# Kernel optimization log

Measured on AMD Instinct MI355X. Metric: run time of the kernel, lower is better.

Reference implementation:

```python
import jax, jax.numpy as jnp
import numpy as np

N_NODES = 100000
N_EDGES = 1600000
IN_C, HID_C, OUT_C = 128, 128, 64


def setup_inputs() -> dict:
    key = jax.random.key(0)
    ks = jax.random.split(key, 6)
    x = jax.random.normal(ks[0], (N_NODES, IN_C), dtype=jnp.float32)
    edge_index = jax.random.randint(ks[1], (2, N_EDGES), 0, N_NODES)
    W1 = jax.random.normal(ks[2], (IN_C, HID_C), dtype=jnp.float32) * (1.0 / np.sqrt(IN_C))
    b1 = jnp.zeros((HID_C,), dtype=jnp.float32)
    W2 = jax.random.normal(ks[3], (HID_C, OUT_C), dtype=jnp.float32) * (1.0 / np.sqrt(HID_C))
    b2 = jnp.zeros((OUT_C,), dtype=jnp.float32)
    return {"x": x, "edge_index": edge_index, "W1": W1, "b1": b1, "W2": W2, "b2": b2}


def gcn_conv(x, W, b, src, dst):
    # PyG GCNConv: D^{-1/2} (A + I) D^{-1/2} X W + b, with self-loops handled
    # analytically (no explicit self-loop edges materialized).
    h = x @ W                                             # [N, d_out]
    ones = jnp.ones(src.shape[0], dtype=h.dtype)
    deg = jax.ops.segment_sum(ones, dst, num_segments=N_NODES) + 1.0  # +1 self-loop
    dinv = jax.lax.rsqrt(deg)                             # deg >= 1, safe
    norm = dinv[src] * dinv[dst]                          # [E]
    msg = h[src] * norm[:, None]                          # gather + scale  [E, d_out]
    agg = jax.ops.segment_sum(msg, dst, num_segments=N_NODES)
    agg = agg + h * (dinv * dinv)[:, None]                # self-loop contribution
    return agg + b


def reference(x, edge_index, W1, b1, W2, b2):
    src, dst = edge_index[0], edge_index[1]
    h = jax.nn.relu(gcn_conv(x, W1, b1, src, dst))
    # dropout is identity in eval mode
    out = gcn_conv(h, W2, b2, src, dst)
    return out
```

## Files before the change

### kernel.cpp

```cpp
#include <hip/hip_runtime.h>

#define N_NODESC 100000
#define N_EDGESC 1600000
#define NB_BUCKETS 391
#define CHUNK_A 8192

typedef __attribute__((ext_vector_type(4))) float floatx4;
typedef __attribute__((ext_vector_type(8))) short shortx8;

__device__ __forceinline__ unsigned short f32_to_bf16_rne(float f) {
    unsigned int u = __float_as_uint(f);
    unsigned int r = u + 0x7fffu + ((u >> 16) & 1u);
    return (unsigned short)(r >> 16);
}
__device__ __forceinline__ float bf16_to_f32(unsigned short h) {
    return __uint_as_float(((unsigned int)h) << 16);
}
__device__ __forceinline__ float bflo(unsigned int u) { return __uint_as_float(u << 16); }
__device__ __forceinline__ float bfhi(unsigned int u) { return __uint_as_float(u & 0xffff0000u); }
__device__ __forceinline__ unsigned int pack2bf(float a, float b) {
    return ((unsigned int)f32_to_bf16_rne(b) << 16) | (unsigned int)f32_to_bf16_rne(a);
}

__global__ __launch_bounds__(256) void k_bcount(const int* __restrict__ dst,
                                                int* __restrict__ bcnt) {
    __shared__ int hist[NB_BUCKETS];
    int t = threadIdx.x;
    for (int i = t; i < NB_BUCKETS; i += 256) hist[i] = 0;
    __syncthreads();
    int base = blockIdx.x * CHUNK_A;
    int end = min(base + CHUNK_A, N_EDGESC);
    for (int e = base + t; e < end; e += 256)
        atomicAdd(&hist[dst[e] >> 8], 1);
    __syncthreads();
    for (int i = t; i < NB_BUCKETS; i += 256)
        if (hist[i] > 0) atomicAdd(&bcnt[i], hist[i]);
}

__global__ __launch_bounds__(512) void k_bscan(const int* __restrict__ bcnt,
                                               int* __restrict__ bstart,
                                               int* __restrict__ gcur) {
    __shared__ int s[512];
    int t = threadIdx.x;
    int v = (t < NB_BUCKETS) ? bcnt[t] : 0;
    s[t] = v;
    __syncthreads();
    int own = v;
    for (int off = 1; off < 512; off <<= 1) {
        int add = (t >= off) ? s[t - off] : 0;
        __syncthreads();
        s[t] += add;
        __syncthreads();
    }
    int excl = s[t] - own;
    if (t < NB_BUCKETS) { bstart[t] = excl; gcur[t] = excl; }
}

__global__ __launch_bounds__(256) void k_bucket(const int* __restrict__ src,
        const int* __restrict__ dst, int* __restrict__ gcur,
        unsigned int* __restrict__ tmp) {
    __shared__ int hist[NB_BUCKETS];
    int t = threadIdx.x;
    for (int i = t; i < NB_BUCKETS; i += 256) hist[i] = 0;
    __syncthreads();
    int base = blockIdx.x * CHUNK_A;
    int end = min(base + CHUNK_A, N_EDGESC);
    for (int e = base + t; e < end; e += 256)
        atomicAdd(&hist[dst[e] >> 8], 1);
    __syncthreads();
    for (int i = t; i < NB_BUCKETS; i += 256) {
        int c = hist[i];
        hist[i] = (c > 0) ? atomicAdd(&gcur[i], c) : 0;
    }
    __syncthreads();
    for (int e = base + t; e < end; e += 256) {
        int d = dst[e];
        int pos = atomicAdd(&hist[d >> 8], 1);
        tmp[pos] = ((unsigned int)src[e] << 8) | (unsigned int)(d & 255);
    }
}

__global__ __launch_bounds__(256) void k_place(const unsigned int* __restrict__ tmp,
        const int* __restrict__ bstart, const int* __restrict__ gcur,
        int* __restrict__ swsrc, int* __restrict__ deg,
        int* __restrict__ row_ptr, float* __restrict__ dinv) {
    __shared__ int hist[256], scan[256], lcur[256];
    int b = blockIdx.x, t = threadIdx.x;
    int start = bstart[b];
    int end = gcur[b];
    hist[t] = 0;
    __syncthreads();
    for (int i = start + t; i < end; i += 256)
        atomicAdd(&hist[tmp[i] & 255u], 1);
    __syncthreads();
    int own = hist[t];
    scan[t] = own;
    __syncthreads();
    for (int off = 1; off < 256; off <<= 1) {
        int add = (t >= off) ? scan[t - off] : 0;
        __syncthreads();
        scan[t] += add;
        __syncthreads();
    }
    int rp = start + scan[t] - own;
    lcur[t] = rp;
    int node = (b << 8) + t;
    if (node < N_NODESC) {
        deg[node] = own;
        row_ptr[node] = rp;
        dinv[node] = rsqrtf((float)own + 1.0f);
    }
    __syncthreads();
    for (int i = start + t; i < end; i += 256) {
        unsigned int v = tmp[i];
        int pos = atomicAdd(&lcur[v & 255u], 1);
        swsrc[pos] = (int)(v >> 8);
    }
}

template<int NOUT>
__global__ void k_wfrag(const float* __restrict__ W,
                        unsigned short* __restrict__ whi, unsigned short* __restrict__ wlo) {
    int idx = blockIdx.x * 256 + threadIdx.x;
    constexpr int C = NOUT / 16;
    int k = idx / NOUT, col = idx % NOUT;
    float f = W[idx];
    unsigned short hi = f32_to_bf16_rne(f);
    unsigned short lo = f32_to_bf16_rne(f - bf16_to_f32(hi));
    int kc = k >> 5, q = (k >> 3) & 3, j = k & 7;
    int c = col >> 4, n = col & 15;
    int o = (((kc * C + c) * 4 + q) * 16 + n) * 8 + j;
    whi[o] = hi; wlo[o] = lo;
}

template<int NOUT, int AFP32>
__global__ __launch_bounds__(256) void k_gemm_mfma(const void* __restrict__ Xv,
        const unsigned short* __restrict__ whi, const unsigned short* __restrict__ wlo,
        const float* __restrict__ dinv, unsigned short* __restrict__ H) {
    constexpr int C = NOUT / 16;
    constexpr int PITCH = NOUT + 4;
    __shared__ __align__(16) float etile[4][16][PITCH];
    int wv = threadIdx.x >> 6, lane = threadIdx.x & 63;
    int n16 = lane & 15, q = lane >> 4;
    int rowBase = blockIdx.x * 128 + wv * 32;
    floatx4 acc[2][C];
#pragma unroll
    for (int m = 0; m < 2; ++m)
#pragma unroll
        for (int c = 0; c < C; ++c) acc[m][c] = (floatx4){0.f, 0.f, 0.f, 0.f};

    const shortx8* whi8 = (const shortx8*)whi;
    const shortx8* wlo8 = (const shortx8*)wlo;

    for (int kc = 0; kc < 4; ++kc) {
        shortx8 ahi[2], alo[2];
#pragma unroll
        for (int m = 0; m < 2; ++m) {
            int r = rowBase + m * 16 + n16;
            if (r >= N_NODESC) r = N_NODESC - 1;
            if (AFP32) {
                const float* xp = &((const float*)Xv)[(size_t)r * 128 + kc * 32 + q * 8];
                floatx4 x0 = *(const floatx4*)xp;
                floatx4 x1 = *(const floatx4*)(xp + 4);
#pragma unroll
                for (int jj = 0; jj < 4; ++jj) {
                    unsigned short h0 = f32_to_bf16_rne(x0[jj]);
                    ahi[m][jj] = (short)h0;
                    alo[m][jj] = (short)f32_to_bf16_rne(x0[jj] - bf16_to_f32(h0));
                    unsigned short h1 = f32_to_bf16_rne(x1[jj]);
                    ahi[m][jj + 4] = (short)h1;
                    alo[m][jj + 4] = (short)f32_to_bf16_rne(x1[jj] - bf16_to_f32(h1));
                }
            } else {
                const unsigned short* xp = &((const unsigned short*)Xv)[(size_t)r * 128 + kc * 32 + q * 8];
                ahi[m] = *(const shortx8*)xp;
            }
        }
#pragma unroll
        for (int c = 0; c < C; ++c) {
            int fo = (kc * C + c) * 64 + lane;
            shortx8 bhi = whi8[fo];
            shortx8 blo = wlo8[fo];
#pragma unroll
            for (int m = 0; m < 2; ++m) {
                acc[m][c] = __builtin_amdgcn_mfma_f32_16x16x32_bf16(ahi[m], bhi, acc[m][c], 0, 0, 0);
                if (AFP32)
                    acc[m][c] = __builtin_amdgcn_mfma_f32_16x16x32_bf16(alo[m], bhi, acc[m][c], 0, 0, 0);
                acc[m][c] = __builtin_amdgcn_mfma_f32_16x16x32_bf16(ahi[m], blo, acc[m][c], 0, 0, 0);
            }
        }
    }
    constexpr int CPL = NOUT / 4;
#pragma unroll
    for (int m = 0; m < 2; ++m) {
        __syncthreads();
#pragma unroll
        for (int c = 0; c < C; ++c)
#pragma unroll
            for (int reg = 0; reg < 4; ++reg)
                etile[wv][q * 4 + reg][c * 16 + n16] = acc[m][c][reg];
        __syncthreads();
        int row = lane >> 2, cb = lane & 3;
        int r = rowBase + m * 16 + row;
        if (r < N_NODESC) {
            float dv = dinv[r];
            unsigned int po[CPL / 2];
#pragma unroll
            for (int i = 0; i < CPL / 4; ++i) {
                floatx4 v = *(const floatx4*)&etile[wv][row][cb * CPL + i * 4];
                po[i * 2 + 0] = pack2bf(v[0] * dv, v[1] * dv);
                po[i * 2 + 1] = pack2bf(v[2] * dv, v[3] * dv);
            }
            unsigned int* op = (unsigned int*)&H[(size_t)r * NOUT + cb * CPL];
#pragma unroll
            for (int i = 0; i < CPL / 8; ++i)
                *(uint4*)(op + i * 4) = *(uint4*)&po[i * 4];
        }
    }
}

__global__ __launch_bounds__(256) void k_agg128(const unsigned short* __restrict__ Hb,
        const int* __restrict__ swsrc, const int* __restrict__ row_ptr,
        const int* __restrict__ deg, const float* __restrict__ dinv,
        const float* __restrict__ bias, unsigned short* __restrict__ outb) {
    int node = blockIdx.x * 4 + (threadIdx.x >> 6);
    int lane = threadIdx.x & 63;
    int g = lane >> 4, l16 = lane & 15;
    int start = row_ptr[node];
    int end = start + deg[node];
    float acc[8] = {0.f, 0.f, 0.f, 0.f, 0.f, 0.f, 0.f, 0.f};
    int j = start + g;
    for (; j + 4 < end; j += 8) {
        int s0 = swsrc[j];
        int s1 = swsrc[j + 4];
        uint4 v0 = *(const uint4*)(Hb + (size_t)s0 * 128 + l16 * 8);
        uint4 v1 = *(const uint4*)(Hb + (size_t)s1 * 128 + l16 * 8);
        acc[0] += bflo(v0.x) + bflo(v1.x);
        acc[1] += bfhi(v0.x) + bfhi(v1.x);
        acc[2] += bflo(v0.y) + bflo(v1.y);
        acc[3] += bfhi(v0.y) + bfhi(v1.y);
        acc[4] += bflo(v0.z) + bflo(v1.z);
        acc[5] += bfhi(v0.z) + bfhi(v1.z);
        acc[6] += bflo(v0.w) + bflo(v1.w);
        acc[7] += bfhi(v0.w) + bfhi(v1.w);
    }
    if (j < end) {
        int s0 = swsrc[j];
        uint4 v0 = *(const uint4*)(Hb + (size_t)s0 * 128 + l16 * 8);
        acc[0] += bflo(v0.x); acc[1] += bfhi(v0.x);
        acc[2] += bflo(v0.y); acc[3] += bfhi(v0.y);
        acc[4] += bflo(v0.z); acc[5] += bfhi(v0.z);
        acc[6] += bflo(v0.w); acc[7] += bfhi(v0.w);
    }
#pragma unroll
    for (int i = 0; i < 8; ++i) {
        acc[i] += __shfl_xor(acc[i], 16);
        acc[i] += __shfl_xor(acc[i], 32);
    }
    if (g == 0) {
        float dv = dinv[node];
        uint4 sv = *(const uint4*)(Hb + (size_t)node * 128 + l16 * 8);
        floatx4 b0 = *(const floatx4*)&bias[l16 * 8];
        floatx4 b1 = *(const floatx4*)&bias[l16 * 8 + 4];
        float o0 = dv * (acc[0] + bflo(sv.x)) + b0[0];
        float o1 = dv * (acc[1] + bfhi(sv.x)) + b0[1];
        float o2 = dv * (acc[2] + bflo(sv.y)) + b0[2];
        float o3 = dv * (acc[3] + bfhi(sv.y)) + b0[3];
        float o4 = dv * (acc[4] + bflo(sv.z)) + b1[0];
        float o5 = dv * (acc[5] + bfhi(sv.z)) + b1[1];
        float o6 = dv * (acc[6] + bflo(sv.w)) + b1[2];
        float o7 = dv * (acc[7] + bfhi(sv.w)) + b1[3];
        uint4 o;
        o.x = pack2bf(fmaxf(o0, 0.f), fmaxf(o1, 0.f));
        o.y = pack2bf(fmaxf(o2, 0.f), fmaxf(o3, 0.f));
        o.z = pack2bf(fmaxf(o4, 0.f), fmaxf(o5, 0.f));
        o.w = pack2bf(fmaxf(o6, 0.f), fmaxf(o7, 0.f));
        *(uint4*)(outb + (size_t)node * 128 + l16 * 8) = o;
    }
}

__global__ __launch_bounds__(256) void k_agg64(const unsigned short* __restrict__ Hb,
        const int* __restrict__ swsrc, const int* __restrict__ row_ptr,
        const int* __restrict__ deg, const float* __restrict__ dinv,
        const float* __restrict__ bias, float* __restrict__ out) {
    int node = blockIdx.x * 4 + (threadIdx.x >> 6);
    int lane = threadIdx.x & 63;
    int g = lane >> 3, l8 = lane & 7;
    int start = row_ptr[node];
    int end = start + deg[node];
    float acc[8] = {0.f, 0.f, 0.f, 0.f, 0.f, 0.f, 0.f, 0.f};
    int j = start + g;
    for (; j + 8 < end; j += 16) {
        int s0 = swsrc[j];
        int s1 = swsrc[j + 8];
        uint4 v0 = *(const uint4*)(Hb + (size_t)s0 * 64 + l8 * 8);
        uint4 v1 = *(const uint4*)(Hb + (size_t)s1 * 64 + l8 * 8);
        acc[0] += bflo(v0.x) + bflo(v1.x);
        acc[1] += bfhi(v0.x) + bfhi(v1.x);
        acc[2] += bflo(v0.y) + bflo(v1.y);
        acc[3] += bfhi(v0.y) + bfhi(v1.y);
        acc[4] += bflo(v0.z) + bflo(v1.z);
        acc[5] += bfhi(v0.z) + bfhi(v1.z);
        acc[6] += bflo(v0.w) + bflo(v1.w);
        acc[7] += bfhi(v0.w) + bfhi(v1.w);
    }
    if (j < end) {
        int s0 = swsrc[j];
        uint4 v0 = *(const uint4*)(Hb + (size_t)s0 * 64 + l8 * 8);
        acc[0] += bflo(v0.x); acc[1] += bfhi(v0.x);
        acc[2] += bflo(v0.y); acc[3] += bfhi(v0.y);
        acc[4] += bflo(v0.z); acc[5] += bfhi(v0.z);
        acc[6] += bflo(v0.w); acc[7] += bfhi(v0.w);
    }
#pragma unroll
    for (int i = 0; i < 8; ++i) {
        acc[i] += __shfl_xor(acc[i], 8);
        acc[i] += __shfl_xor(acc[i], 16);
        acc[i] += __shfl_xor(acc[i], 32);
    }
    if (g == 0) {
        float dv = dinv[node];
        uint4 sv = *(const uint4*)(Hb + (size_t)node * 64 + l8 * 8);
        floatx4 b0 = *(const floatx4*)&bias[l8 * 8];
        floatx4 b1 = *(const floatx4*)&bias[l8 * 8 + 4];
        floatx4 o0, o1;
        o0[0] = dv * (acc[0] + bflo(sv.x)) + b0[0];
        o0[1] = dv * (acc[1] + bfhi(sv.x)) + b0[1];
        o0[2] = dv * (acc[2] + bflo(sv.y)) + b0[2];
        o0[3] = dv * (acc[3] + bfhi(sv.y)) + b0[3];
        o1[0] = dv * (acc[4] + bflo(sv.z)) + b1[0];
        o1[1] = dv * (acc[5] + bfhi(sv.z)) + b1[1];
        o1[2] = dv * (acc[6] + bflo(sv.w)) + b1[2];
        o1[3] = dv * (acc[7] + bfhi(sv.w)) + b1[3];
        *(floatx4*)&out[(size_t)node * 64 + l8 * 8] = o0;
        *(floatx4*)&out[(size_t)node * 64 + l8 * 8 + 4] = o1;
    }
}

extern "C" void kernel_launch(void* const* d_in, const int* in_sizes, int n_in,
                              void* d_out, int out_size, void* d_ws, size_t ws_size,
                              hipStream_t stream) {
    const float* x  = (const float*)d_in[0];
    const int*   ei = (const int*)d_in[1];
    const float* W1 = (const float*)d_in[2];
    const float* b1 = (const float*)d_in[3];
    const float* W2 = (const float*)d_in[4];
    const float* b2 = (const float*)d_in[5];
    float* out = (float*)d_out;
    const int* src = ei;
    const int* dst = ei + N_EDGESC;

    char* ws = (char*)d_ws;
    size_t off = 0;
    auto alloc = [&](size_t bytes) -> void* {
        off = (off + 255) & ~(size_t)255;
        void* p = ws + off;
        off += bytes;
        return p;
    };
    int*   deg     = (int*)  alloc((size_t)N_NODESC * 4);
    float* dinv    = (float*)alloc((size_t)N_NODESC * 4);
    int*   row_ptr = (int*)  alloc((size_t)N_NODESC * 4);
    int*   bcnt    = (int*)  alloc(NB_BUCKETS * 4);
    int*   bstart  = (int*)  alloc(NB_BUCKETS * 4);
    int*   gcur    = (int*)  alloc(NB_BUCKETS * 4);
    unsigned int* tmp   = (unsigned int*)alloc((size_t)N_EDGESC * 4);
    int*   swsrc   = (int*)  alloc((size_t)N_EDGESC * 4);
    unsigned short* w1hi = (unsigned short*)alloc(128 * 128 * 2);
    unsigned short* w1lo = (unsigned short*)alloc(128 * 128 * 2);
    unsigned short* w2hi = (unsigned short*)alloc(128 * 64 * 2);
    unsigned short* w2lo = (unsigned short*)alloc(128 * 64 * 2);
    unsigned short* h1b  = (unsigned short*)alloc((size_t)N_NODESC * 128 * 2);
    unsigned short* hb   = (unsigned short*)alloc((size_t)N_NODESC * 128 * 2);
    unsigned short* h2b  = h1b;

    const int nbGemm = (N_NODESC + 127) / 128;
    const int nbBkt  = (N_EDGESC + CHUNK_A - 1) / CHUNK_A;

    hipMemsetAsync(bcnt, 0, NB_BUCKETS * 4, stream);
    k_bcount<<<nbBkt, 256, 0, stream>>>(dst, bcnt);
    k_bscan<<<1, 512, 0, stream>>>(bcnt, bstart, gcur);
    k_bucket<<<nbBkt, 256, 0, stream>>>(src, dst, gcur, tmp);
    k_place<<<NB_BUCKETS, 256, 0, stream>>>(tmp, bstart, gcur, swsrc, deg, row_ptr, dinv);

    k_wfrag<128><<<(128 * 128) / 256, 256, 0, stream>>>(W1, w1hi, w1lo);
    k_wfrag<64><<<(128 * 64) / 256, 256, 0, stream>>>(W2, w2hi, w2lo);

    k_gemm_mfma<128, 1><<<nbGemm, 256, 0, stream>>>(x, w1hi, w1lo, dinv, h1b);
    k_agg128<<<N_NODESC / 4, 256, 0, stream>>>(h1b, swsrc, row_ptr, deg, dinv, b1, hb);
    k_gemm_mfma<64, 0><<<nbGemm, 256, 0, stream>>>(hb, w2hi, w2lo, dinv, h2b);
    k_agg64<<<N_NODESC / 4, 256, 0, stream>>>(h2b, swsrc, row_ptr, deg, dinv, b2, out);
}
```

Before: 311.1 us.

## Slice aggregation by feature columns so concurrent blocks share a narrow gather working set

Both sparse aggregation kernels are rewritten so each block covers 32 nodes and one 16-column slice of the features, with 8 threads per node each loading 4 bytes per edge. Previously one wavefront gathered a node's full row in 16-byte pieces. With consecutive blocks assigned to different column slices, the set of rows being gathered at one time touches only a narrow band of columns. The aim is better cache locality for the random gathers. The cost is many more small 4-byte loads, repeated index reads across slices, and sequential per-thread edge loops with no cross-lane reduction.

```diff
diff --git a/kernel.cpp b/kernel.cpp
--- a/kernel.cpp
+++ b/kernel.cpp
@@ -6,6 +6,7 @@
 #define CHUNK_A 8192
 
 typedef __attribute__((ext_vector_type(4))) float floatx4;
+typedef __attribute__((ext_vector_type(2))) float floatx2;
 typedef __attribute__((ext_vector_type(8))) short shortx8;
 
 __device__ __forceinline__ unsigned short f32_to_bf16_rne(float f) {
@@ -219,122 +220,80 @@
     }
 }
 
-__global__ __launch_bounds__(256) void k_agg128(const unsigned short* __restrict__ Hb,
+__global__ __launch_bounds__(256) void k_agg128s(const unsigned short* __restrict__ Hb,
         const int* __restrict__ swsrc, const int* __restrict__ row_ptr,
         const int* __restrict__ deg, const float* __restrict__ dinv,
         const float* __restrict__ bias, unsigned short* __restrict__ outb) {
-    int node = blockIdx.x * 4 + (threadIdx.x >> 6);
-    int lane = threadIdx.x & 63;
-    int g = lane >> 4, l16 = lane & 15;
+    int slice = blockIdx.x & 7;
+    int nb = blockIdx.x >> 3;
+    int grp = threadIdx.x >> 3;
+    int l8 = threadIdx.x & 7;
+    int node = nb * 32 + grp;
+    int colOff = slice * 16 + l8 * 2;
+    const unsigned short* Hc = Hb + colOff;
     int start = row_ptr[node];
     int end = start + deg[node];
-    float acc[8] = {0.f, 0.f, 0.f, 0.f, 0.f, 0.f, 0.f, 0.f};
-    int j = start + g;
-    for (; j + 4 < end; j += 8) {
-        int s0 = swsrc[j];
-        int s1 = swsrc[j + 4];
-        uint4 v0 = *(const uint4*)(Hb + (size_t)s0 * 128 + l16 * 8);
-        uint4 v1 = *(const uint4*)(Hb + (size_t)s1 * 128 + l16 * 8);
-        acc[0] += bflo(v0.x) + bflo(v1.x);
-        acc[1] += bfhi(v0.x) + bfhi(v1.x);
-        acc[2] += bflo(v0.y) + bflo(v1.y);
-        acc[3] += bfhi(v0.y) + bfhi(v1.y);
-        acc[4] += bflo(v0.z) + bflo(v1.z);
-        acc[5] += bfhi(v0.z) + bfhi(v1.z);
-        acc[6] += bflo(v0.w) + bflo(v1.w);
-        acc[7] += bfhi(v0.w) + bfhi(v1.w);
-    }
-    if (j < end) {
-        int s0 = swsrc[j];
-        uint4 v0 = *(const uint4*)(Hb + (size_t)s0 * 128 + l16 * 8);
-        acc[0] += bflo(v0.x); acc[1] += bfhi(v0.x);
-        acc[2] += bflo(v0.y); acc[3] += bfhi(v0.y);
-        acc[4] += bflo(v0.z); acc[5] += bfhi(v0.z);
-        acc[6] += bflo(v0.w); acc[7] += bfhi(v0.w);
-    }
-#pragma unroll
-    for (int i = 0; i < 8; ++i) {
-        acc[i] += __shfl_xor(acc[i], 16);
-        acc[i] += __shfl_xor(acc[i], 32);
-    }
-    if (g == 0) {
-        float dv = dinv[node];
-        uint4 sv = *(const uint4*)(Hb + (size_t)node * 128 + l16 * 8);
-        floatx4 b0 = *(const floatx4*)&bias[l16 * 8];
-        floatx4 b1 = *(const floatx4*)&bias[l16 * 8 + 4];
-        float o0 = dv * (acc[0] + bflo(sv.x)) + b0[0];
-        float o1 = dv * (acc[1] + bfhi(sv.x)) + b0[1];
-        float o2 = dv * (acc[2] + bflo(sv.y)) + b0[2];
-        float o3 = dv * (acc[3] + bfhi(sv.y)) + b0[3];
-        float o4 = dv * (acc[4] + bflo(sv.z)) + b1[0];
-        float o5 = dv * (acc[5] + bfhi(sv.z)) + b1[1];
-        float o6 = dv * (acc[6] + bflo(sv.w)) + b1[2];
-        float o7 = dv * (acc[7] + bfhi(sv.w)) + b1[3];
-        uint4 o;
-        o.x = pack2bf(fmaxf(o0, 0.f), fmaxf(o1, 0.f));
-        o.y = pack2bf(fmaxf(o2, 0.f), fmaxf(o3, 0.f));
-        o.z = pack2bf(fmaxf(o4, 0.f), fmaxf(o5, 0.f));
-        o.w = pack2bf(fmaxf(o6, 0.f), fmaxf(o7, 0.f));
-        *(uint4*)(outb + (size_t)node * 128 + l16 * 8) = o;
-    }
-}
-
-__global__ __launch_bounds__(256) void k_agg64(const unsigned short* __restrict__ Hb,
+    float a0 = 0.f, a1 = 0.f;
+    int j = start;
+    for (; j + 3 < end; j += 4) {
+        int s0 = swsrc[j], s1 = swsrc[j + 1], s2 = swsrc[j + 2], s3 = swsrc[j + 3];
+        unsigned int v0 = *(const unsigned int*)(Hc + (size_t)s0 * 128);
+        unsigned int v1 = *(const unsigned int*)(Hc + (size_t)s1 * 128);
+        unsigned int v2 = *(const unsigned int*)(Hc + (size_t)s2 * 128);
+        unsigned int v3 = *(const unsigned int*)(Hc + (size_t)s3 * 128);
+        a0 += bflo(v0) + bflo(v1) + bflo(v2) + bflo(v3);
+        a1 += bfhi(v0) + bfhi(v1) + bfhi(v2) + bfhi(v3);
+    }
+    for (; j < end; ++j) {
+        unsigned int v0 = *(const unsigned int*)(Hc + (size_t)swsrc[j] * 128);
+        a0 += bflo(v0); a1 += bfhi(v0);
+    }
+    float dv = dinv[node];
+    unsigned int sv = *(const unsigned int*)(Hc + (size_t)node * 128);
+    float o0 = dv * (a0 + bflo(sv)) + bias[colOff];
+    float o1 = dv * (a1 + bfhi(sv)) + bias[colOff + 1];
+    *(unsigned int*)(outb + (size_t)node * 128 + colOff) =
+        pack2bf(fmaxf(o0, 0.f), fmaxf(o1, 0.f));
+}
+
+#define NBH64 1563
+__global__ __launch_bounds__(256) void k_agg64s(const unsigned short* __restrict__ Hb,
         const int* __restrict__ swsrc, const int* __restrict__ row_ptr,
         const int* __restrict__ deg, const float* __restrict__ dinv,
         const float* __restrict__ bias, float* __restrict__ out) {
-    int node = blockIdx.x * 4 + (threadIdx.x >> 6);
-    int lane = threadIdx.x & 63;
-    int g = lane >> 3, l8 = lane & 7;
+    int x = blockIdx.x & 7;
+    int slice = x & 3;
+    int half = x >> 2;
+    int nb = (blockIdx.x >> 3) + half * NBH64;
+    int grp = threadIdx.x >> 3;
+    int l8 = threadIdx.x & 7;
+    int node = nb * 32 + grp;
+    if (node >= N_NODESC) return;
+    int colOff = slice * 16 + l8 * 2;
+    const unsigned short* Hc = Hb + colOff;
     int start = row_ptr[node];
     int end = start + deg[node];
-    float acc[8] = {0.f, 0.f, 0.f, 0.f, 0.f, 0.f, 0.f, 0.f};
-    int j = start + g;
-    for (; j + 8 < end; j += 16) {
-        int s0 = swsrc[j];
-        int s1 = swsrc[j + 8];
-        uint4 v0 = *(const uint4*)(Hb + (size_t)s0 * 64 + l8 * 8);
-        uint4 v1 = *(const uint4*)(Hb + (size_t)s1 * 64 + l8 * 8);
-        acc[0] += bflo(v0.x) + bflo(v1.x);
-        acc[1] += bfhi(v0.x) + bfhi(v1.x);
-        acc[2] += bflo(v0.y) + bflo(v1.y);
-        acc[3] += bfhi(v0.y) + bfhi(v1.y);
-        acc[4] += bflo(v0.z) + bflo(v1.z);
-        acc[5] += bfhi(v0.z) + bfhi(v1.z);
-        acc[6] += bflo(v0.w) + bflo(v1.w);
-        acc[7] += bfhi(v0.w) + bfhi(v1.w);
-    }
-    if (j < end) {
-        int s0 = swsrc[j];
-        uint4 v0 = *(const uint4*)(Hb + (size_t)s0 * 64 + l8 * 8);
-        acc[0] += bflo(v0.x); acc[1] += bfhi(v0.x);
-        acc[2] += bflo(v0.y); acc[3] += bfhi(v0.y);
-        acc[4] += bflo(v0.z); acc[5] += bfhi(v0.z);
-        acc[6] += bflo(v0.w); acc[7] += bfhi(v0.w);
-    }
-#pragma unroll
-    for (int i = 0; i < 8; ++i) {
-        acc[i] += __shfl_xor(acc[i], 8);
-        acc[i] += __shfl_xor(acc[i], 16);
-        acc[i] += __shfl_xor(acc[i], 32);
-    }
-    if (g == 0) {
-        float dv = dinv[node];
-        uint4 sv = *(const uint4*)(Hb + (size_t)node * 64 + l8 * 8);
-        floatx4 b0 = *(const floatx4*)&bias[l8 * 8];
-        floatx4 b1 = *(const floatx4*)&bias[l8 * 8 + 4];
-        floatx4 o0, o1;
-        o0[0] = dv * (acc[0] + bflo(sv.x)) + b0[0];
-        o0[1] = dv * (acc[1] + bfhi(sv.x)) + b0[1];
-        o0[2] = dv * (acc[2] + bflo(sv.y)) + b0[2];
-        o0[3] = dv * (acc[3] + bfhi(sv.y)) + b0[3];
-        o1[0] = dv * (acc[4] + bflo(sv.z)) + b1[0];
-        o1[1] = dv * (acc[5] + bfhi(sv.z)) + b1[1];
-        o1[2] = dv * (acc[6] + bflo(sv.w)) + b1[2];
-        o1[3] = dv * (acc[7] + bfhi(sv.w)) + b1[3];
-        *(floatx4*)&out[(size_t)node * 64 + l8 * 8] = o0;
-        *(floatx4*)&out[(size_t)node * 64 + l8 * 8 + 4] = o1;
-    }
+    float a0 = 0.f, a1 = 0.f;
+    int j = start;
+    for (; j + 3 < end; j += 4) {
+        int s0 = swsrc[j], s1 = swsrc[j + 1], s2 = swsrc[j + 2], s3 = swsrc[j + 3];
+        unsigned int v0 = *(const unsigned int*)(Hc + (size_t)s0 * 64);
+        unsigned int v1 = *(const unsigned int*)(Hc + (size_t)s1 * 64);
+        unsigned int v2 = *(const unsigned int*)(Hc + (size_t)s2 * 64);
+        unsigned int v3 = *(const unsigned int*)(Hc + (size_t)s3 * 64);
+        a0 += bflo(v0) + bflo(v1) + bflo(v2) + bflo(v3);
+        a1 += bfhi(v0) + bfhi(v1) + bfhi(v2) + bfhi(v3);
+    }
+    for (; j < end; ++j) {
+        unsigned int v0 = *(const unsigned int*)(Hc + (size_t)swsrc[j] * 64);
+        a0 += bflo(v0); a1 += bfhi(v0);
+    }
+    float dv = dinv[node];
+    unsigned int sv = *(const unsigned int*)(Hc + (size_t)node * 64);
+    floatx2 o;
+    o[0] = dv * (a0 + bflo(sv)) + bias[colOff];
+    o[1] = dv * (a1 + bfhi(sv)) + bias[colOff + 1];
+    *(floatx2*)&out[(size_t)node * 64 + colOff] = o;
 }
 
 extern "C" void kernel_launch(void* const* d_in, const int* in_sizes, int n_in,
@@ -387,7 +346,7 @@
     k_wfrag<64><<<(128 * 64) / 256, 256, 0, stream>>>(W2, w2hi, w2lo);
 
     k_gemm_mfma<128, 1><<<nbGemm, 256, 0, stream>>>(x, w1hi, w1lo, dinv, h1b);
-    k_agg128<<<N_NODESC / 4, 256, 0, stream>>>(h1b, swsrc, row_ptr, deg, dinv, b1, hb);
+    k_agg128s<<<(N_NODESC / 32) * 8, 256, 0, stream>>>(h1b, swsrc, row_ptr, deg, dinv, b1, hb);
     k_gemm_mfma<64, 0><<<nbGemm, 256, 0, stream>>>(hb, w2hi, w2lo, dinv, h2b);
-    k_agg64<<<N_NODESC / 4, 256, 0, stream>>>(h2b, swsrc, row_ptr, deg, dinv, b2, out);
-}
+    k_agg64s<<<NBH64 * 8, 256, 0, stream>>>(h2b, swsrc, row_ptr, deg, dinv, b2, out);
+}
```

After: 498.6 us. 1.6x slower.
